# Performance work log

Hardware: AMD Instinct MI355X
Metric: run time of the kernel (lower is better)

The kernel has to match this reference:

```python
import jax, jax.numpy as jnp
import numpy as np

VOCAB = 32000
EMB = 300
DEC_UNITS = 512
UNITS = 2 * DEC_UNITS        # GRU units = 1024
ENC_DIM = 1024               # encoder output feature dim
B, S = 256, 128
IN_DIM = ENC_DIM + EMB       # GRU input: [context ; embedding] = 1324


def setup_inputs() -> dict:
    key = jax.random.key(0)
    ks = jax.random.split(key, 16)
    sc = 0.02
    return {
        "x": jax.random.randint(ks[0], (B, 1), 0, VOCAB),
        "state": jax.random.normal(ks[1], (B, UNITS), jnp.float32),
        "encoder_output": jax.random.normal(ks[2], (B, S, ENC_DIM), jnp.float32),
        "emb": jax.random.normal(ks[3], (VOCAB, EMB), jnp.float32) * sc,
        "W1": jax.random.normal(ks[4], (ENC_DIM, DEC_UNITS), jnp.float32) * sc,
        "b1": jnp.zeros((DEC_UNITS,), jnp.float32),
        "W2": jax.random.normal(ks[5], (UNITS, DEC_UNITS), jnp.float32) * sc,
        "b2": jnp.zeros((DEC_UNITS,), jnp.float32),
        "V": jax.random.normal(ks[6], (DEC_UNITS, 1), jnp.float32) * sc,
        "bV": jnp.zeros((1,), jnp.float32),
        "gru_k": jax.random.normal(ks[7], (IN_DIM, 3 * UNITS), jnp.float32) * sc,
        "gru_rk": jax.random.normal(ks[8], (UNITS, 3 * UNITS), jnp.float32) * sc,
        "gru_b": jnp.zeros((2, 3 * UNITS), jnp.float32),  # [input_bias, recurrent_bias] (reset_after=True)
        "fc_W": jax.random.normal(ks[9], (UNITS, VOCAB), jnp.float32) * sc,
        "fc_b": jnp.zeros((VOCAB,), jnp.float32),
    }


def reference(x, state, encoder_output, emb, W1, b1, W2, b2, V, bV,
              gru_k, gru_rk, gru_b, fc_W, fc_b):
    # --- Bahdanau attention (query = state, values = encoder_output) ---
    # score: [B, S, 1]
    q = state @ W2 + b2                                    # [B, U_att]
    score = jnp.tanh(encoder_output @ W1 + b1 + q[:, None, :]) @ V + bV
    attn = jax.nn.softmax(score, axis=1)                   # [B, S, 1]
    context = jnp.sum(attn * encoder_output, axis=1)       # [B, ENC_DIM]

    # --- embed token and concat with context (seq len 1) ---
    x_emb = emb[x[:, 0]]                                   # [B, EMB]
    xi = jnp.concatenate([context, x_emb], axis=-1)        # [B, IN_DIM]

    # --- single GRU step (Keras GRU, reset_after=True, inference: no dropout) ---
    mx = xi @ gru_k + gru_b[0]                             # [B, 3U]
    mh = state @ gru_rk + gru_b[1]                         # [B, 3U]
    xz, xr, xh = jnp.split(mx, 3, axis=-1)
    hz, hr, hh_rec = jnp.split(mh, 3, axis=-1)
    z = jax.nn.sigmoid(xz + hz)
    r = jax.nn.sigmoid(xr + hr)
    hh = jnp.tanh(xh + r * hh_rec)
    h = z * state + (1.0 - z) * hh                         # [B, UNITS]

    # --- softmax projection over vocab ---
    probs = jax.nn.softmax(h @ fc_W + fc_b, axis=-1)       # [B, VOCAB]
    return probs, h, attn
```

## Files before the change

kernel.cpp:

```cpp
#include <hip/hip_runtime.h>
#include <math.h>

#define B_    256
#define S_    128
#define ENCD  1024
#define DECU  512
#define UNITS 1024
#define VOCAB 32000
#define EMB_  300
#define INDIM 1324
#define KPADX 1344
#define G3    3072

typedef __bf16 bf16x8 __attribute__((ext_vector_type(8)));
typedef __bf16 bf16x4 __attribute__((ext_vector_type(4)));
typedef __bf16 bf16x2 __attribute__((ext_vector_type(2)));
typedef float  f32x4  __attribute__((ext_vector_type(4)));

#define MFMA16(a, b, c) __builtin_amdgcn_mfma_f32_16x16x32_bf16((a), (b), (c), 0, 0, 0)

__device__ __forceinline__ int swz(int row, int e) { return row * 64 + (e ^ ((row & 7) << 3)); }

__device__ __forceinline__ float fast_tanh(float x) {
  x = fminf(fmaxf(x, -15.f), 15.f);
  float e = __expf(2.f * x);
  return (e - 1.f) / (e + 1.f);
}

__global__ __launch_bounds__(256) void k_cvt_state(const float* __restrict__ in,
                                                   __bf16* __restrict__ out) {
  int i4 = blockIdx.x * 256 + threadIdx.x;
  float4 f = *(const float4*)(in + (size_t)i4 * 4);
  bf16x4 o = {(__bf16)f.x, (__bf16)f.y, (__bf16)f.z, (__bf16)f.w};
  *(bf16x4*)(out + (size_t)i4 * 4) = o;
}

__global__ __launch_bounds__(1024) void k_w1t(const float* __restrict__ W1,
                                              __bf16* __restrict__ W1t) {
  int n = blockIdx.x;
  int k = threadIdx.x;
  W1t[(size_t)n * 1024 + k] = (__bf16)W1[(size_t)k * 512 + n];
}

template <int BM>
__global__ __launch_bounds__(512) void k_gemm(const __bf16* __restrict__ A, int ldaK,
                                              const float* __restrict__ B,
                                              const float* __restrict__ bias,
                                              float* __restrict__ C, int K, int N) {
  constexpr int WR = (BM == 256) ? 4 : 2;
  constexpr int WN = 8 / WR;
  constexpr int MI = BM / (WR * 16);
  constexpr int NI = 64 / (WN * 16);
  __shared__ __align__(16) __bf16 As[BM * 64];
  __shared__ __align__(16) __bf16 Bs[64 * 64];
  int tid = threadIdx.x, lane = tid & 63, w = tid >> 6;
  int wr = (BM == 256) ? (w >> 1) : (w >> 2);
  int wn = (BM == 256) ? (w & 1) : (w & 3);
  int m0 = blockIdx.x * BM, n0 = blockIdx.y * 64;
  int lrow = lane & 15, lk = (lane >> 4) * 8;
  int r0 = wr * MI * 16, c0 = wn * NI * 16;
  f32x4 acc[MI][NI] = {};

  constexpr int ACH = (BM == 256) ? 4 : 1;
  bf16x8 pfa[ACH];
  float pfb[8];
  int am = (BM == 256) ? (tid >> 1) : (tid >> 3);
  int aks = (BM == 256) ? ((tid & 1) * 32) : ((tid & 7) * 8);
  const __bf16* arow = A + (size_t)(m0 + am) * ldaK + aks;
  int bn = tid & 63, bks = (tid >> 6) * 8;

  int nk = (K + 63) >> 6;
#pragma unroll
  for (int c = 0; c < ACH; ++c) pfa[c] = *(const bf16x8*)(arow + c * 8);
#pragma unroll
  for (int i = 0; i < 8; ++i) { int k = bks + i; pfb[i] = (k < K) ? B[(size_t)k * N + n0 + bn] : 0.f; }

  for (int it = 0; it < nk; ++it) {
#pragma unroll
    for (int c = 0; c < ACH; ++c) *(bf16x8*)&As[swz(am, aks + c * 8)] = pfa[c];
    {
      __bf16 tb[8];
#pragma unroll
      for (int i = 0; i < 8; ++i) tb[i] = (__bf16)pfb[i];
      *(bf16x8*)&Bs[swz(bn, bks)] = *(bf16x8*)&tb[0];
    }
    __syncthreads();
    if (it + 1 < nk) {
      int k0 = (it + 1) * 64;
#pragma unroll
      for (int c = 0; c < ACH; ++c) pfa[c] = *(const bf16x8*)(arow + k0 + c * 8);
#pragma unroll
      for (int i = 0; i < 8; ++i) { int k = k0 + bks + i; pfb[i] = (k < K) ? B[(size_t)k * N + n0 + bn] : 0.f; }
    }
#pragma unroll
    for (int kk = 0; kk < 64; kk += 32) {
      bf16x8 av[MI], bv[NI];
#pragma unroll
      for (int mi = 0; mi < MI; ++mi) { int r = r0 + mi * 16 + lrow; av[mi] = *(bf16x8*)&As[swz(r, kk + lk)]; }
#pragma unroll
      for (int ni = 0; ni < NI; ++ni) { int r = c0 + ni * 16 + lrow; bv[ni] = *(bf16x8*)&Bs[swz(r, kk + lk)]; }
#pragma unroll
      for (int mi = 0; mi < MI; ++mi)
#pragma unroll
        for (int ni = 0; ni < NI; ++ni) acc[mi][ni] = MFMA16(av[mi], bv[ni], acc[mi][ni]);
    }
    __syncthreads();
  }
#pragma unroll
  for (int mi = 0; mi < MI; ++mi)
#pragma unroll
    for (int ni = 0; ni < NI; ++ni) {
      int colg = n0 + c0 + ni * 16 + lrow;
      float bvv = bias[colg];
#pragma unroll
      for (int reg = 0; reg < 4; ++reg) {
        int rowg = m0 + r0 + mi * 16 + (lane >> 4) * 4 + reg;
        C[(size_t)rowg * N + colg] = acc[mi][ni][reg] + bvv;
      }
    }
}

__global__ __launch_bounds__(512) void k_attn_fused(const float* __restrict__ enc,
                                                    const __bf16* __restrict__ W1t,
                                                    const float* __restrict__ b1,
                                                    const float* __restrict__ q,
                                                    const float* __restrict__ V,
                                                    const float* __restrict__ bV,
                                                    const int* __restrict__ x,
                                                    const float* __restrict__ emb,
                                                    float* __restrict__ attn_out,
                                                    __bf16* __restrict__ xi_bf) {
  __shared__ __align__(16) __bf16 As[128 * 64];
  __shared__ __align__(16) __bf16 Bs[512 * 64];
  __shared__ float sc_p[4][128];
  __shared__ float sc_s[128];
  __shared__ float aw_s[128];
  int b = blockIdx.x;
  int tid = threadIdx.x, lane = tid & 63, w = tid >> 6;
  int wr = w >> 2, wn = w & 3;
  int lrow = lane & 15, lk = (lane >> 4) * 8;
  f32x4 acc[4][8] = {};

  float4 pfa[4];
  bf16x8 pfb[8];
  int am = tid >> 2, aks = (tid & 3) * 16;
  const float* arow = enc + ((size_t)b * 128 + am) * ENCD + aks;
  int bn = tid >> 3, bks = (tid & 7) * 8;
  {
    pfa[0] = *(const float4*)arow; pfa[1] = *(const float4*)(arow + 4);
    pfa[2] = *(const float4*)(arow + 8); pfa[3] = *(const float4*)(arow + 12);
#pragma unroll
    for (int j = 0; j < 8; ++j)
      pfb[j] = *(const bf16x8*)(W1t + (size_t)(bn + 64 * j) * 1024 + bks);
  }
  for (int it = 0; it < 16; ++it) {
    __bf16 tmp[16];
#pragma unroll
    for (int v = 0; v < 4; ++v) {
      tmp[v * 4 + 0] = (__bf16)pfa[v].x; tmp[v * 4 + 1] = (__bf16)pfa[v].y;
      tmp[v * 4 + 2] = (__bf16)pfa[v].z; tmp[v * 4 + 3] = (__bf16)pfa[v].w;
    }
    *(bf16x8*)&As[swz(am, aks)]     = *(bf16x8*)&tmp[0];
    *(bf16x8*)&As[swz(am, aks + 8)] = *(bf16x8*)&tmp[8];
#pragma unroll
    for (int j = 0; j < 8; ++j) *(bf16x8*)&Bs[swz(bn + 64 * j, bks)] = pfb[j];
    __syncthreads();
    if (it + 1 < 16) {
      int k0 = (it + 1) * 64;
      const float* p = arow + k0;
      pfa[0] = *(const float4*)p; pfa[1] = *(const float4*)(p + 4);
      pfa[2] = *(const float4*)(p + 8); pfa[3] = *(const float4*)(p + 12);
#pragma unroll
      for (int j = 0; j < 8; ++j)
        pfb[j] = *(const bf16x8*)(W1t + (size_t)(bn + 64 * j) * 1024 + k0 + bks);
    }
#pragma unroll
    for (int kk = 0; kk < 64; kk += 32) {
      bf16x8 av[4], bv[8];
#pragma unroll
      for (int mi = 0; mi < 4; ++mi) { int r = wr * 64 + mi * 16 + lrow; av[mi] = *(bf16x8*)&As[swz(r, kk + lk)]; }
#pragma unroll
      for (int ni = 0; ni < 8; ++ni) { int r = wn * 128 + ni * 16 + lrow; bv[ni] = *(bf16x8*)&Bs[swz(r, kk + lk)]; }
#pragma unroll
      for (int mi = 0; mi < 4; ++mi)
#pragma unroll
        for (int ni = 0; ni < 8; ++ni) acc[mi][ni] = MFMA16(av[mi], bv[ni], acc[mi][ni]);
    }
    __syncthreads();
  }
  float psum[4][4] = {};
#pragma unroll
  for (int mi = 0; mi < 4; ++mi)
#pragma unroll
    for (int ni = 0; ni < 8; ++ni) {
      int j = wn * 128 + ni * 16 + lrow;
      float vj = V[j], b1j = b1[j], qv = q[(size_t)b * DECU + j];
#pragma unroll
      for (int reg = 0; reg < 4; ++reg)
        psum[mi][reg] += vj * fast_tanh(acc[mi][ni][reg] + b1j + qv);
    }
#pragma unroll
  for (int off = 1; off < 16; off <<= 1)
#pragma unroll
    for (int mi = 0; mi < 4; ++mi)
#pragma unroll
      for (int reg = 0; reg < 4; ++reg)
        psum[mi][reg] += __shfl_xor(psum[mi][reg], off);
  if (lrow == 0) {
#pragma unroll
    for (int mi = 0; mi < 4; ++mi)
#pragma unroll
      for (int reg = 0; reg < 4; ++reg) {
        int rl = wr * 64 + mi * 16 + (lane >> 4) * 4 + reg;
        sc_p[wn][rl] = psum[mi][reg];
      }
  }
  __syncthreads();
  if (tid < S_) sc_s[tid] = bV[0] + sc_p[0][tid] + sc_p[1][tid] + sc_p[2][tid] + sc_p[3][tid];
  __syncthreads();
  float mx = -INFINITY;
  for (int s = 0; s < S_; ++s) mx = fmaxf(mx, sc_s[s]);
  float sum = 0.f;
  for (int s = 0; s < S_; ++s) sum += __expf(sc_s[s] - mx);
  float inv = 1.f / sum;
  if (tid < S_) {
    float av = __expf(sc_s[tid] - mx) * inv;
    aw_s[tid] = av;
    attn_out[(size_t)b * S_ + tid] = av;
  }
  __syncthreads();
  int c = tid * 2;
  float ax = 0.f, ay = 0.f;
  const float* eb = enc + (size_t)b * S_ * ENCD + c;
#pragma unroll 8
  for (int s = 0; s < S_; ++s) {
    float2 e = *(const float2*)(eb + (size_t)s * ENCD);
    float av = aw_s[s];
    ax = fmaf(av, e.x, ax);
    ay = fmaf(av, e.y, ay);
  }
  bf16x2 o = {(__bf16)ax, (__bf16)ay};
  *(bf16x2*)&xi_bf[(size_t)b * KPADX + c] = o;
  int xb = x[b];
  if (tid < 75) {
    float4 f = *(const float4*)&emb[(size_t)xb * EMB_ + tid * 4];
    bf16x4 o4 = {(__bf16)f.x, (__bf16)f.y, (__bf16)f.z, (__bf16)f.w};
    *(bf16x4*)&xi_bf[(size_t)b * KPADX + ENCD + tid * 4] = o4;
  } else if (tid < 80) {
    bf16x4 z = {(__bf16)0.f, (__bf16)0.f, (__bf16)0.f, (__bf16)0.f};
    *(bf16x4*)&xi_bf[(size_t)b * KPADX + INDIM + (tid - 75) * 4] = z;
  }
}

__global__ __launch_bounds__(256) void k_gates(const float* __restrict__ mx,
                                               const float* __restrict__ mh,
                                               const float* __restrict__ state,
                                               float* __restrict__ h_out,
                                               __bf16* __restrict__ h_bf) {
  int idx = blockIdx.x * 256 + threadIdx.x;
  int b = idx >> 10, j = idx & 1023;
  const float* mxr = mx + (size_t)b * G3;
  const float* mhr = mh + (size_t)b * G3;
  float z = 1.f / (1.f + __expf(-(mxr[j] + mhr[j])));
  float r = 1.f / (1.f + __expf(-(mxr[UNITS + j] + mhr[UNITS + j])));
  float hh = tanhf(mxr[2 * UNITS + j] + r * mhr[2 * UNITS + j]);
  float st = state[idx];
  float h = z * st + (1.f - z) * hh;
  h_out[idx] = h;
  h_bf[idx] = (__bf16)h;
}

__global__ __launch_bounds__(1024) void k_softmax(float* __restrict__ logits) {
  int b = blockIdx.x, t = threadIdx.x;
  int lane = t & 63, w = t >> 6;
  float4* row4 = (float4*)(logits + (size_t)b * VOCAB);
  __shared__ float redm[16];
  __shared__ float reds[16];
  float4 v[8];
  float m = -INFINITY;
#pragma unroll
  for (int i = 0; i < 8; ++i) {
    int i4 = i * 1024 + t;
    if (i4 < 8000) {
      v[i] = row4[i4];
      m = fmaxf(m, fmaxf(fmaxf(v[i].x, v[i].y), fmaxf(v[i].z, v[i].w)));
    } else {
      v[i] = make_float4(-INFINITY, -INFINITY, -INFINITY, -INFINITY);
    }
  }
#pragma unroll
  for (int o = 32; o >= 1; o >>= 1) m = fmaxf(m, __shfl_xor(m, o));
  if (lane == 0) redm[w] = m;
  __syncthreads();
  float m2 = -INFINITY;
#pragma unroll
  for (int i = 0; i < 16; ++i) m2 = fmaxf(m2, redm[i]);
  float s = 0.f;
#pragma unroll
  for (int i = 0; i < 8; ++i) {
    v[i].x = __expf(v[i].x - m2);
    v[i].y = __expf(v[i].y - m2);
    v[i].z = __expf(v[i].z - m2);
    v[i].w = __expf(v[i].w - m2);
    s += v[i].x + v[i].y + v[i].z + v[i].w;
  }
#pragma unroll
  for (int o = 32; o >= 1; o >>= 1) s += __shfl_xor(s, o);
  if (lane == 0) reds[w] = s;
  __syncthreads();
  float s2 = 0.f;
#pragma unroll
  for (int i = 0; i < 16; ++i) s2 += reds[i];
  float inv = 1.f / s2;
#pragma unroll
  for (int i = 0; i < 8; ++i) {
    int i4 = i * 1024 + t;
    if (i4 < 8000)
      row4[i4] = make_float4(v[i].x * inv, v[i].y * inv, v[i].z * inv, v[i].w * inv);
  }
}

extern "C" void kernel_launch(void* const* d_in, const int* in_sizes, int n_in,
                              void* d_out, int out_size, void* d_ws, size_t ws_size,
                              hipStream_t stream) {
  const int*   x     = (const int*)d_in[0];
  const float* state = (const float*)d_in[1];
  const float* enc   = (const float*)d_in[2];
  const float* emb   = (const float*)d_in[3];
  const float* W1    = (const float*)d_in[4];
  const float* b1    = (const float*)d_in[5];
  const float* W2    = (const float*)d_in[6];
  const float* b2    = (const float*)d_in[7];
  const float* V     = (const float*)d_in[8];
  const float* bV    = (const float*)d_in[9];
  const float* gru_k = (const float*)d_in[10];
  const float* gru_rk= (const float*)d_in[11];
  const float* gru_b = (const float*)d_in[12];
  const float* fc_W  = (const float*)d_in[13];
  const float* fc_b  = (const float*)d_in[14];

  float* out   = (float*)d_out;
  float* probs = out;
  float* h_out = out + (size_t)B_ * VOCAB;
  float* attn  = h_out + (size_t)B_ * UNITS;

  float* ws = (float*)d_ws;
  float* q  = ws;
  float* mx = q + (size_t)B_ * DECU;
  float* mh = mx + (size_t)B_ * G3;
  __bf16* state_bf = (__bf16*)(mh + (size_t)B_ * G3);
  __bf16* xi_bf    = state_bf + (size_t)B_ * UNITS;
  __bf16* h_bf     = xi_bf + (size_t)B_ * KPADX;
  __bf16* W1t      = h_bf + (size_t)B_ * UNITS;

  k_cvt_state<<<256, 256, 0, stream>>>(state, state_bf);
  k_w1t<<<512, 1024, 0, stream>>>(W1, W1t);
  k_gemm<64><<<dim3(4, 8), 512, 0, stream>>>(state_bf, UNITS, W2, b2, q, UNITS, DECU);
  k_attn_fused<<<B_, 512, 0, stream>>>(enc, W1t, b1, q, V, bV, x, emb, attn, xi_bf);
  k_gemm<64><<<dim3(4, 48), 512, 0, stream>>>(xi_bf, KPADX, gru_k, gru_b, mx, INDIM, G3);
  k_gemm<64><<<dim3(4, 48), 512, 0, stream>>>(state_bf, UNITS, gru_rk, gru_b + G3, mh, UNITS, G3);
  k_gates<<<(B_ * UNITS) / 256, 256, 0, stream>>>(mx, mh, state, h_out, h_bf);
  k_gemm<256><<<dim3(1, VOCAB / 64), 512, 0, stream>>>(h_bf, UNITS, fc_W, fc_b, probs, UNITS, VOCAB);
  k_softmax<<<B_, 1024, 0, stream>>>(probs);
}
```

Measured before the change: 205.3 us.

## Split attention kernel into N-tiled score kernel and separate softmax/context kernel

The fused attention kernel, which had one 512-thread block per batch row covering all 512 attention units, is split in two. A score kernel runs a 256x4 grid, each block computing a 128-unit slice of the tanh/V score and writing partial sums to workspace. A second kernel reduces the partials, applies the softmax and computes the context with float4 loads. This gives four times as many blocks with smaller LDS and register footprints for better occupancy. In exchange it drops the register prefetch double-buffering, re-reads the encoder tile four times, and adds a launch plus a workspace round trip.

```diff
diff --git a/kernel.cpp b/kernel.cpp
--- a/kernel.cpp
+++ b/kernel.cpp
@@ -120,71 +120,62 @@
     }
 }
 
-__global__ __launch_bounds__(512) void k_attn_fused(const float* __restrict__ enc,
-                                                    const __bf16* __restrict__ W1t,
-                                                    const float* __restrict__ b1,
-                                                    const float* __restrict__ q,
-                                                    const float* __restrict__ V,
-                                                    const float* __restrict__ bV,
-                                                    const int* __restrict__ x,
-                                                    const float* __restrict__ emb,
-                                                    float* __restrict__ attn_out,
-                                                    __bf16* __restrict__ xi_bf) {
+__global__ __launch_bounds__(256) void k_score2(const float* __restrict__ enc,
+                                                const __bf16* __restrict__ W1t,
+                                                const float* __restrict__ b1,
+                                                const float* __restrict__ q,
+                                                const float* __restrict__ V,
+                                                float* __restrict__ sc_part) {
   __shared__ __align__(16) __bf16 As[128 * 64];
-  __shared__ __align__(16) __bf16 Bs[512 * 64];
-  __shared__ float sc_p[4][128];
-  __shared__ float sc_s[128];
-  __shared__ float aw_s[128];
-  int b = blockIdx.x;
+  __shared__ __align__(16) __bf16 Bs[128 * 64];
+  __shared__ float red[2][128];
+  int b = blockIdx.x, by = blockIdx.y;
+  int n0 = by * 128;
   int tid = threadIdx.x, lane = tid & 63, w = tid >> 6;
-  int wr = w >> 2, wn = w & 3;
+  int wr = w >> 1, wn = w & 1;
   int lrow = lane & 15, lk = (lane >> 4) * 8;
-  f32x4 acc[4][8] = {};
-
-  float4 pfa[4];
-  bf16x8 pfb[8];
-  int am = tid >> 2, aks = (tid & 3) * 16;
-  const float* arow = enc + ((size_t)b * 128 + am) * ENCD + aks;
-  int bn = tid >> 3, bks = (tid & 7) * 8;
-  {
-    pfa[0] = *(const float4*)arow; pfa[1] = *(const float4*)(arow + 4);
-    pfa[2] = *(const float4*)(arow + 8); pfa[3] = *(const float4*)(arow + 12);
-#pragma unroll
-    for (int j = 0; j < 8; ++j)
-      pfb[j] = *(const bf16x8*)(W1t + (size_t)(bn + 64 * j) * 1024 + bks);
-  }
+  int r0 = wr * 64, c0 = wn * 64;
+  f32x4 acc[4][4] = {};
+
+  int am = tid >> 1, aks = (tid & 1) * 32;
+  const float* ap0 = enc + ((size_t)b * 128 + am) * ENCD + aks;
+  int bn = tid >> 1, bks = (tid & 1) * 32;
+  const __bf16* bp0 = W1t + (size_t)(n0 + bn) * 1024 + bks;
+
   for (int it = 0; it < 16; ++it) {
-    __bf16 tmp[16];
-#pragma unroll
-    for (int v = 0; v < 4; ++v) {
-      tmp[v * 4 + 0] = (__bf16)pfa[v].x; tmp[v * 4 + 1] = (__bf16)pfa[v].y;
-      tmp[v * 4 + 2] = (__bf16)pfa[v].z; tmp[v * 4 + 3] = (__bf16)pfa[v].w;
-    }
-    *(bf16x8*)&As[swz(am, aks)]     = *(bf16x8*)&tmp[0];
-    *(bf16x8*)&As[swz(am, aks + 8)] = *(bf16x8*)&tmp[8];
-#pragma unroll
-    for (int j = 0; j < 8; ++j) *(bf16x8*)&Bs[swz(bn + 64 * j, bks)] = pfb[j];
+    int k0 = it * 64;
+    {
+      const float* ap = ap0 + k0;
+      float4 f[8];
+#pragma unroll
+      for (int c = 0; c < 8; ++c) f[c] = *(const float4*)(ap + c * 4);
+      __bf16 t[32];
+#pragma unroll
+      for (int c = 0; c < 8; ++c) {
+        t[c * 4 + 0] = (__bf16)f[c].x; t[c * 4 + 1] = (__bf16)f[c].y;
+        t[c * 4 + 2] = (__bf16)f[c].z; t[c * 4 + 3] = (__bf16)f[c].w;
+      }
+#pragma unroll
+      for (int c = 0; c < 4; ++c) *(bf16x8*)&As[swz(am, aks + c * 8)] = *(bf16x8*)&t[c * 8];
+    }
+    {
+      const __bf16* bp = bp0 + k0;
+#pragma unroll
+      for (int c = 0; c < 4; ++c)
+        *(bf16x8*)&Bs[swz(bn, bks + c * 8)] = *(const bf16x8*)(bp + c * 8);
+    }
     __syncthreads();
-    if (it + 1 < 16) {
-      int k0 = (it + 1) * 64;
-      const float* p = arow + k0;
-      pfa[0] = *(const float4*)p; pfa[1] = *(const float4*)(p + 4);
-      pfa[2] = *(const float4*)(p + 8); pfa[3] = *(const float4*)(p + 12);
-#pragma unroll
-      for (int j = 0; j < 8; ++j)
-        pfb[j] = *(const bf16x8*)(W1t + (size_t)(bn + 64 * j) * 1024 + k0 + bks);
-    }
 #pragma unroll
     for (int kk = 0; kk < 64; kk += 32) {
-      bf16x8 av[4], bv[8];
-#pragma unroll
-      for (int mi = 0; mi < 4; ++mi) { int r = wr * 64 + mi * 16 + lrow; av[mi] = *(bf16x8*)&As[swz(r, kk + lk)]; }
-#pragma unroll
-      for (int ni = 0; ni < 8; ++ni) { int r = wn * 128 + ni * 16 + lrow; bv[ni] = *(bf16x8*)&Bs[swz(r, kk + lk)]; }
+      bf16x8 av[4], bv[4];
+#pragma unroll
+      for (int mi = 0; mi < 4; ++mi) { int r = r0 + mi * 16 + lrow; av[mi] = *(bf16x8*)&As[swz(r, kk + lk)]; }
+#pragma unroll
+      for (int ni = 0; ni < 4; ++ni) { int r = c0 + ni * 16 + lrow; bv[ni] = *(bf16x8*)&Bs[swz(r, kk + lk)]; }
 #pragma unroll
       for (int mi = 0; mi < 4; ++mi)
 #pragma unroll
-        for (int ni = 0; ni < 8; ++ni) acc[mi][ni] = MFMA16(av[mi], bv[ni], acc[mi][ni]);
+        for (int ni = 0; ni < 4; ++ni) acc[mi][ni] = MFMA16(av[mi], bv[ni], acc[mi][ni]);
     }
     __syncthreads();
   }
@@ -192,8 +183,8 @@
 #pragma unroll
   for (int mi = 0; mi < 4; ++mi)
 #pragma unroll
-    for (int ni = 0; ni < 8; ++ni) {
-      int j = wn * 128 + ni * 16 + lrow;
+    for (int ni = 0; ni < 4; ++ni) {
+      int j = n0 + c0 + ni * 16 + lrow;
       float vj = V[j], b1j = b1[j], qv = q[(size_t)b * DECU + j];
 #pragma unroll
       for (int reg = 0; reg < 4; ++reg)
@@ -210,45 +201,60 @@
 #pragma unroll
     for (int mi = 0; mi < 4; ++mi)
 #pragma unroll
-      for (int reg = 0; reg < 4; ++reg) {
-        int rl = wr * 64 + mi * 16 + (lane >> 4) * 4 + reg;
-        sc_p[wn][rl] = psum[mi][reg];
-      }
-  }
-  __syncthreads();
-  if (tid < S_) sc_s[tid] = bV[0] + sc_p[0][tid] + sc_p[1][tid] + sc_p[2][tid] + sc_p[3][tid];
+      for (int reg = 0; reg < 4; ++reg)
+        red[wn][r0 + mi * 16 + (lane >> 4) * 4 + reg] = psum[mi][reg];
+  }
+  __syncthreads();
+  if (tid < 128)
+    sc_part[((size_t)b * 128 + tid) * 4 + by] = red[0][tid] + red[1][tid];
+}
+
+__global__ __launch_bounds__(256) void k_attn_ctx2(const float* __restrict__ sc_part,
+                                                   const float* __restrict__ bV,
+                                                   const float* __restrict__ enc,
+                                                   const int* __restrict__ x,
+                                                   const float* __restrict__ emb,
+                                                   float* __restrict__ attn_out,
+                                                   __bf16* __restrict__ xi_bf) {
+  int b = blockIdx.x, t = threadIdx.x;
+  __shared__ float a_s[S_];
+  if (t < S_) {
+    float4 p = *(const float4*)&sc_part[((size_t)b * 128 + t) * 4];
+    a_s[t] = bV[0] + p.x + p.y + p.z + p.w;
+  }
   __syncthreads();
   float mx = -INFINITY;
-  for (int s = 0; s < S_; ++s) mx = fmaxf(mx, sc_s[s]);
+  for (int s = 0; s < S_; ++s) mx = fmaxf(mx, a_s[s]);
   float sum = 0.f;
-  for (int s = 0; s < S_; ++s) sum += __expf(sc_s[s] - mx);
+  for (int s = 0; s < S_; ++s) sum += __expf(a_s[s] - mx);
   float inv = 1.f / sum;
-  if (tid < S_) {
-    float av = __expf(sc_s[tid] - mx) * inv;
-    aw_s[tid] = av;
-    attn_out[(size_t)b * S_ + tid] = av;
-  }
-  __syncthreads();
-  int c = tid * 2;
-  float ax = 0.f, ay = 0.f;
+  __syncthreads();
+  if (t < S_) {
+    float av = __expf(a_s[t] - mx) * inv;
+    a_s[t] = av;
+    attn_out[(size_t)b * S_ + t] = av;
+  }
+  __syncthreads();
+  int c = t * 4;
+  float a0 = 0.f, a1 = 0.f, a2 = 0.f, a3 = 0.f;
   const float* eb = enc + (size_t)b * S_ * ENCD + c;
 #pragma unroll 8
   for (int s = 0; s < S_; ++s) {
-    float2 e = *(const float2*)(eb + (size_t)s * ENCD);
-    float av = aw_s[s];
-    ax = fmaf(av, e.x, ax);
-    ay = fmaf(av, e.y, ay);
-  }
-  bf16x2 o = {(__bf16)ax, (__bf16)ay};
-  *(bf16x2*)&xi_bf[(size_t)b * KPADX + c] = o;
+    float4 e = *(const float4*)(eb + (size_t)s * ENCD);
+    float av = a_s[s];
+    a0 = fmaf(av, e.x, a0); a1 = fmaf(av, e.y, a1);
+    a2 = fmaf(av, e.z, a2); a3 = fmaf(av, e.w, a3);
+  }
+  bf16x4 o = {(__bf16)a0, (__bf16)a1, (__bf16)a2, (__bf16)a3};
+  *(bf16x4*)&xi_bf[(size_t)b * KPADX + c] = o;
   int xb = x[b];
-  if (tid < 75) {
-    float4 f = *(const float4*)&emb[(size_t)xb * EMB_ + tid * 4];
+  if (t < 75) {
+    float4 f = *(const float4*)&emb[(size_t)xb * EMB_ + t * 4];
     bf16x4 o4 = {(__bf16)f.x, (__bf16)f.y, (__bf16)f.z, (__bf16)f.w};
-    *(bf16x4*)&xi_bf[(size_t)b * KPADX + ENCD + tid * 4] = o4;
-  } else if (tid < 80) {
+    *(bf16x4*)&xi_bf[(size_t)b * KPADX + ENCD + t * 4] = o4;
+  } else if (t < 80) {
     bf16x4 z = {(__bf16)0.f, (__bf16)0.f, (__bf16)0.f, (__bf16)0.f};
-    *(bf16x4*)&xi_bf[(size_t)b * KPADX + INDIM + (tid - 75) * 4] = z;
+    *(bf16x4*)&xi_bf[(size_t)b * KPADX + INDIM + (t - 75) * 4] = z;
   }
 }
 
@@ -345,9 +351,10 @@
   float* attn  = h_out + (size_t)B_ * UNITS;
 
   float* ws = (float*)d_ws;
-  float* q  = ws;
-  float* mx = q + (size_t)B_ * DECU;
-  float* mh = mx + (size_t)B_ * G3;
+  float* q       = ws;
+  float* sc_part = q + (size_t)B_ * DECU;
+  float* mx      = sc_part + (size_t)B_ * S_ * 4;
+  float* mh      = mx + (size_t)B_ * G3;
   __bf16* state_bf = (__bf16*)(mh + (size_t)B_ * G3);
   __bf16* xi_bf    = state_bf + (size_t)B_ * UNITS;
   __bf16* h_bf     = xi_bf + (size_t)B_ * KPADX;
@@ -356,7 +363,8 @@
   k_cvt_state<<<256, 256, 0, stream>>>(state, state_bf);
   k_w1t<<<512, 1024, 0, stream>>>(W1, W1t);
   k_gemm<64><<<dim3(4, 8), 512, 0, stream>>>(state_bf, UNITS, W2, b2, q, UNITS, DECU);
-  k_attn_fused<<<B_, 512, 0, stream>>>(enc, W1t, b1, q, V, bV, x, emb, attn, xi_bf);
+  k_score2<<<dim3(B_, 4), 256, 0, stream>>>(enc, W1t, b1, q, V, sc_part);
+  k_attn_ctx2<<<B_, 256, 0, stream>>>(sc_part, bV, enc, x, emb, attn, xi_bf);
   k_gemm<64><<<dim3(4, 48), 512, 0, stream>>>(xi_bf, KPADX, gru_k, gru_b, mx, INDIM, G3);
   k_gemm<64><<<dim3(4, 48), 512, 0, stream>>>(state_bf, UNITS, gru_rk, gru_b + G3, mh, UNITS, G3);
   k_gates<<<(B_ * UNITS) / 256, 256, 0, stream>>>(mx, mh, state, h_out, h_bf);
```

Result: slower. 259.9 us (+26.6%).
